# Optimization experiments

Measured on AMD Instinct MI355X. Metric: run time of the kernel, lower is better.

## Reference

```python
import jax, jax.numpy as jnp
import numpy as np

N_NODES = 20000
N_EDGES = 320000
DIMS = [256, 256, 128, 64]  # input_dim, hidden_dims...
EPS = 1e-5


def gcn_conv(x, w, b, src, dst, n):
    # PyG GCNConv: linear first, then symmetric-normalized aggregation with self-loops
    x = x @ w  # [N, out]
    loops = jnp.arange(n, dtype=src.dtype)
    src2 = jnp.concatenate([src, loops])
    dst2 = jnp.concatenate([dst, loops])
    deg = jax.ops.segment_sum(jnp.ones_like(dst2, dtype=x.dtype), dst2, num_segments=n)
    dinv = jnp.where(deg > 0, deg ** -0.5, 0.0)
    norm = dinv[src2] * dinv[dst2]  # [E+N]
    msg = x[src2] * norm[:, None]   # gathered, scaled messages
    out = jax.ops.segment_sum(msg, dst2, num_segments=n)
    return out + b


def graph_norm(x, w, b, a):
    # PyG GraphNorm over a single graph: per-feature mean/var across nodes
    mean = jnp.mean(x, axis=0)
    centered = x - a * mean
    var = jnp.mean(centered * centered, axis=0)
    return w * centered * jax.lax.rsqrt(var + EPS) + b


def layer_norm(x, w, b):
    mean = jnp.mean(x, axis=-1, keepdims=True)
    var = jnp.mean((x - mean) ** 2, axis=-1, keepdims=True)
    return (x - mean) * jax.lax.rsqrt(var + EPS) * w + b


def setup_inputs() -> dict:
    key = jax.random.key(0)
    ks = jax.random.split(key, 32)
    inp = {}
    inp["x"] = jax.random.normal(ks[0], (N_NODES, DIMS[0]), dtype=jnp.float32)
    inp["edge_index"] = jax.random.randint(ks[1], (2, N_EDGES), 0, N_NODES, dtype=jnp.int32)
    ki = 2
    for i in range(3):
        fin, fout = DIMS[i], DIMS[i + 1]
        s = 1.0 / np.sqrt(fin)
        inp[f"w{i}"] = jax.random.uniform(ks[ki], (fin, fout), jnp.float32, -s, s); ki += 1
        inp[f"b{i}"] = jnp.zeros((fout,), jnp.float32)
        inp[f"gn{i}_w"] = jnp.ones((fout,), jnp.float32)
        inp[f"gn{i}_b"] = jnp.zeros((fout,), jnp.float32)
        inp[f"gn{i}_a"] = jnp.ones((fout,), jnp.float32)
    h = DIMS[-1]
    s = 1.0 / np.sqrt(3 * h)
    inp["wc1"] = jax.random.uniform(ks[ki], (3 * h, h), jnp.float32, -s, s); ki += 1
    inp["bc1"] = jnp.zeros((h,), jnp.float32)
    inp["ln_w"] = jnp.ones((h,), jnp.float32)
    inp["ln_b"] = jnp.zeros((h,), jnp.float32)
    s = 1.0 / np.sqrt(h)
    inp["wc2"] = jax.random.uniform(ks[ki], (h, 2), jnp.float32, -s, s); ki += 1
    inp["bc2"] = jnp.zeros((2,), jnp.float32)
    return inp


def reference(x, edge_index,
              w0, b0, gn0_w, gn0_b, gn0_a,
              w1, b1, gn1_w, gn1_b, gn1_a,
              w2, b2, gn2_w, gn2_b, gn2_a,
              wc1, bc1, ln_w, ln_b, wc2, bc2):
    src, dst = edge_index[0], edge_index[1]
    n = x.shape[0]
    params = [(w0, b0, gn0_w, gn0_b, gn0_a),
              (w1, b1, gn1_w, gn1_b, gn1_a),
              (w2, b2, gn2_w, gn2_b, gn2_a)]
    for (w, b, gw, gb, ga) in params:
        x_res = x
        x = gcn_conv(x, w, b, src, dst, n)
        x = graph_norm(x, gw, gb, ga)
        x = jax.nn.gelu(x, approximate=False)
        # dropout = identity (eval); residual only when shapes match (layer 0)
        if x.shape == x_res.shape:
            x = x + x_res
    # multi-pool over the single graph (batch vector of zeros): mean | max | sum
    pooled = jnp.concatenate([jnp.mean(x, axis=0), jnp.max(x, axis=0), jnp.sum(x, axis=0)])[None, :]  # [1, 3h]
    h = pooled @ wc1 + bc1
    h = layer_norm(h, ln_w, ln_b)
    h = jax.nn.gelu(h, approximate=False)
    return h @ wc2 + bc2  # [1, num_classes]
```

## Files before the change

### kernel.cpp

```cpp
#include <hip/hip_runtime.h>
#include <math.h>

#define EPSV 1e-5f
#define MAXB 2560
#define GBLK 2080

__device__ __forceinline__ float gelu_f(float x) {
    return 0.5f * x * (1.0f + erff(x * 0.70710678118654752440f));
}

__device__ __forceinline__ float4 f4add(float4 a, float4 b) {
    return make_float4(a.x + b.x, a.y + b.y, a.z + b.z, a.w + b.w);
}

__global__ void deg_kernel(const int* __restrict__ ei, int* __restrict__ deg, int E) {
    int stride = gridDim.x * blockDim.x;
    for (int e = blockIdx.x * blockDim.x + threadIdx.x; e < E; e += stride)
        atomicAdd(&deg[ei[E + e]], 1);
}

__global__ void dinv_kernel(const int* __restrict__ deg, float* __restrict__ dinv, int N) {
    int i = blockIdx.x * blockDim.x + threadIdx.x;
    if (i < N) dinv[i] = rsqrtf((float)(deg[i] + 1));
}

__global__ __launch_bounds__(1024) void scan_kernel(const int* __restrict__ deg,
                                                    int* __restrict__ off, int N) {
    __shared__ int sh[1024];
    int t = threadIdx.x;
    int chunk = (N + 1023) >> 10;
    int b = t * chunk;
    int e = b + chunk; if (e > N) e = N;
    int s = 0;
    for (int i = b; i < e; ++i) s += deg[i];
    sh[t] = s;
    __syncthreads();
    for (int d = 1; d < 1024; d <<= 1) {
        int v = (t >= d) ? sh[t - d] : 0;
        __syncthreads();
        sh[t] += v;
        __syncthreads();
    }
    int run = (t > 0) ? sh[t - 1] : 0;
    for (int i = b; i < e; ++i) { off[i] = run; run += deg[i]; }
    if (t == 1023) off[N] = sh[1023];
}

__global__ void fill_kernel(const int* __restrict__ ei, const int* __restrict__ off,
                            int* __restrict__ fill, int* __restrict__ csr, int E) {
    int stride = gridDim.x * blockDim.x;
    for (int e = blockIdx.x * blockDim.x + threadIdx.x; e < E; e += stride) {
        int d = ei[E + e];
        int p = off[d] + atomicAdd(&fill[d], 1);
        csr[p] = ei[e];
    }
}

__global__ __launch_bounds__(256) void gemm_scale_kernel(
    const float* __restrict__ A, const float* __restrict__ W,
    const float* __restrict__ dinv, float* __restrict__ C,
    int M, int K, int Nc)
{
    __shared__ float As[64][17];
    __shared__ float4 Ws4[16][16];
    const int tid = threadIdx.x;
    const int tx = tid & 15, ty = tid >> 4;
    const int row0 = blockIdx.y * 64, col0 = blockIdx.x * 64;
    float acc[4][4] = {};
    const int ar = tid >> 2, ac4 = (tid & 3) * 4;
    const int wr = tid >> 4, wc4 = (tid & 15) * 4;

    for (int kk = 0; kk < K; kk += 16) {
        float4 av = make_float4(0.f, 0.f, 0.f, 0.f);
        int grow = row0 + ar;
        if (grow < M) av = *(const float4*)(A + (long)grow * K + kk + ac4);
        As[ar][ac4 + 0] = av.x; As[ar][ac4 + 1] = av.y;
        As[ar][ac4 + 2] = av.z; As[ar][ac4 + 3] = av.w;
        Ws4[wr][tid & 15] = *(const float4*)(W + (long)(kk + wr) * Nc + col0 + wc4);
        __syncthreads();
#pragma unroll
        for (int k = 0; k < 16; ++k) {
            float4 b4 = Ws4[k][tx];
            float a0 = As[ty * 4 + 0][k];
            float a1 = As[ty * 4 + 1][k];
            float a2 = As[ty * 4 + 2][k];
            float a3 = As[ty * 4 + 3][k];
            acc[0][0] = fmaf(a0, b4.x, acc[0][0]); acc[0][1] = fmaf(a0, b4.y, acc[0][1]);
            acc[0][2] = fmaf(a0, b4.z, acc[0][2]); acc[0][3] = fmaf(a0, b4.w, acc[0][3]);
            acc[1][0] = fmaf(a1, b4.x, acc[1][0]); acc[1][1] = fmaf(a1, b4.y, acc[1][1]);
            acc[1][2] = fmaf(a1, b4.z, acc[1][2]); acc[1][3] = fmaf(a1, b4.w, acc[1][3]);
            acc[2][0] = fmaf(a2, b4.x, acc[2][0]); acc[2][1] = fmaf(a2, b4.y, acc[2][1]);
            acc[2][2] = fmaf(a2, b4.z, acc[2][2]); acc[2][3] = fmaf(a2, b4.w, acc[2][3]);
            acc[3][0] = fmaf(a3, b4.x, acc[3][0]); acc[3][1] = fmaf(a3, b4.y, acc[3][1]);
            acc[3][2] = fmaf(a3, b4.z, acc[3][2]); acc[3][3] = fmaf(a3, b4.w, acc[3][3]);
        }
        __syncthreads();
    }
#pragma unroll
    for (int i = 0; i < 4; ++i) {
        int grow = row0 + ty * 4 + i;
        if (grow < M) {
            float dv = dinv[grow];
            float4 o = make_float4(acc[i][0] * dv, acc[i][1] * dv, acc[i][2] * dv, acc[i][3] * dv);
            *(float4*)(C + (long)grow * Nc + col0 + tx * 4) = o;
        }
    }
}

template<int F>
__global__ __launch_bounds__(256) void gather_kernel(
    const float* __restrict__ hs, const int* __restrict__ off,
    const int* __restrict__ csr, const float* __restrict__ dinv,
    const float* __restrict__ bias, float* __restrict__ t,
    float* __restrict__ p1, float* __restrict__ p2, int N)
{
    constexpr int NG  = F / 64;
    constexpr int LDR = F / 4;
    constexpr int NPB = 16;
    const int lane = threadIdx.x & 15;
    const int slot = threadIdx.x >> 4;

    const int xs    = blockIdx.x & 7;
    const int g     = xs % NG;
    const int r     = xs / NG;
    const int chunk = blockIdx.x >> 3;
    const int repl  = 8 / NG;
    const int nPerG = (int)(gridDim.x >> 3) * repl;
    const int j     = chunk * repl + r;

    const int col4 = g * 16 + lane;
    const float4* hs4 = (const float4*)hs;
    float4* t4 = (float4*)t;
    const float4 bv = ((const float4*)bias)[col4];

    float4 a1 = make_float4(0.f, 0.f, 0.f, 0.f);
    float4 a2 = make_float4(0.f, 0.f, 0.f, 0.f);

    for (int d = j * NPB + slot; d < N; d += nPerG * NPB) {
        float4 acc = hs4[(long)d * LDR + col4];
        const int e0 = off[d], e1 = off[d + 1];
        int e = e0;
        for (; e + 8 <= e1; e += 8) {
            int s0 = csr[e + 0], s1 = csr[e + 1], s2 = csr[e + 2], s3 = csr[e + 3];
            int s4 = csr[e + 4], s5 = csr[e + 5], s6 = csr[e + 6], s7 = csr[e + 7];
            float4 v0 = hs4[(long)s0 * LDR + col4];
            float4 v1 = hs4[(long)s1 * LDR + col4];
            float4 v2 = hs4[(long)s2 * LDR + col4];
            float4 v3 = hs4[(long)s3 * LDR + col4];
            float4 v4 = hs4[(long)s4 * LDR + col4];
            float4 v5 = hs4[(long)s5 * LDR + col4];
            float4 v6 = hs4[(long)s6 * LDR + col4];
            float4 v7 = hs4[(long)s7 * LDR + col4];
            float4 u0 = f4add(v0, v1);
            float4 u1 = f4add(v2, v3);
            float4 u2 = f4add(v4, v5);
            float4 u3 = f4add(v6, v7);
            acc = f4add(acc, f4add(f4add(u0, u1), f4add(u2, u3)));
        }
        for (; e + 2 <= e1; e += 2) {
            int s0 = csr[e + 0], s1 = csr[e + 1];
            acc = f4add(acc, f4add(hs4[(long)s0 * LDR + col4], hs4[(long)s1 * LDR + col4]));
        }
        if (e < e1) {
            acc = f4add(acc, hs4[(long)csr[e] * LDR + col4]);
        }

        float dv = dinv[d];
        float4 o;
        o.x = fmaf(dv, acc.x, bv.x);
        o.y = fmaf(dv, acc.y, bv.y);
        o.z = fmaf(dv, acc.z, bv.z);
        o.w = fmaf(dv, acc.w, bv.w);
        t4[(long)d * LDR + col4] = o;
        a1.x += o.x; a1.y += o.y; a1.z += o.z; a1.w += o.w;
        a2.x += o.x * o.x; a2.y += o.y * o.y; a2.z += o.z * o.z; a2.w += o.w * o.w;
    }

    __shared__ float red[8][256];
    red[0][threadIdx.x] = a1.x; red[1][threadIdx.x] = a1.y;
    red[2][threadIdx.x] = a1.z; red[3][threadIdx.x] = a1.w;
    red[4][threadIdx.x] = a2.x; red[5][threadIdx.x] = a2.y;
    red[6][threadIdx.x] = a2.z; red[7][threadIdx.x] = a2.w;
    __syncthreads();
    if (slot == 0) {
        float sum[8];
#pragma unroll
        for (int k = 0; k < 8; ++k) {
            float s = red[k][lane];
            for (int jj = 1; jj < NPB; ++jj) s += red[k][jj * 16 + lane];
            sum[k] = s;
        }
        ((float4*)p1)[(long)col4 * MAXB + blockIdx.x] = make_float4(sum[0], sum[1], sum[2], sum[3]);
        ((float4*)p2)[(long)col4 * MAXB + blockIdx.x] = make_float4(sum[4], sum[5], sum[6], sum[7]);
    }
}

__global__ __launch_bounds__(256) void statreduce_kernel(
    const float* __restrict__ p1, const float* __restrict__ p2,
    const float* __restrict__ ga,
    float* __restrict__ meanv, float* __restrict__ istdv,
    int nb, int N, int NG)
{
    const int c4 = blockIdx.x;
    const int g = (c4 >> 4) % NG;
    const float4* p14 = (const float4*)p1 + (long)c4 * MAXB;
    const float4* p24 = (const float4*)p2 + (long)c4 * MAXB;
    float4 a1 = make_float4(0.f, 0.f, 0.f, 0.f);
    float4 a2 = make_float4(0.f, 0.f, 0.f, 0.f);
    for (int r = threadIdx.x; r < nb; r += 256) {
        if (((r & 7) % NG) != g) continue;
        float4 v1 = p14[r];
        float4 v2 = p24[r];
        a1.x += v1.x; a1.y += v1.y; a1.z += v1.z; a1.w += v1.w;
        a2.x += v2.x; a2.y += v2.y; a2.z += v2.z; a2.w += v2.w;
    }
#pragma unroll
    for (int offv = 32; offv > 0; offv >>= 1) {
        a1.x += __shfl_down(a1.x, offv); a1.y += __shfl_down(a1.y, offv);
        a1.z += __shfl_down(a1.z, offv); a1.w += __shfl_down(a1.w, offv);
        a2.x += __shfl_down(a2.x, offv); a2.y += __shfl_down(a2.y, offv);
        a2.z += __shfl_down(a2.z, offv); a2.w += __shfl_down(a2.w, offv);
    }
    __shared__ float4 sh1[4], sh2[4];
    const int wid = threadIdx.x >> 6;
    if ((threadIdx.x & 63) == 0) { sh1[wid] = a1; sh2[wid] = a2; }
    __syncthreads();
    if (threadIdx.x == 0) {
        float4 t1 = sh1[0], t2 = sh2[0];
        for (int jj = 1; jj < 4; ++jj) {
            float4 u1 = sh1[jj], u2 = sh2[jj];
            t1.x += u1.x; t1.y += u1.y; t1.z += u1.z; t1.w += u1.w;
            t2.x += u2.x; t2.y += u2.y; t2.z += u2.z; t2.w += u2.w;
        }
        float s1a[4] = { t1.x, t1.y, t1.z, t1.w };
        float s2a[4] = { t2.x, t2.y, t2.z, t2.w };
#pragma unroll
        for (int k = 0; k < 4; ++k) {
            int c = c4 * 4 + k;
            float m = s1a[k] / (float)N;
            float a = ga[c];
            float var = s2a[k] / (float)N - 2.f * a * m * m + a * a * m * m;
            meanv[c] = m;
            istdv[c] = rsqrtf(var + EPSV);
        }
    }
}

__global__ __launch_bounds__(256) void normgelu_kernel(
    const float* __restrict__ t, const float* __restrict__ meanv,
    const float* __restrict__ istdv, const float* __restrict__ gw,
    const float* __restrict__ gb, const float* __restrict__ ga,
    const float* __restrict__ res, float* __restrict__ out,
    int log2f, long total)
{
    long stride = (long)gridDim.x * blockDim.x;
    int fmask = (1 << log2f) - 1;
    for (long idx = (long)blockIdx.x * blockDim.x + threadIdx.x; idx < total; idx += stride) {
        int c = (int)idx & fmask;
        float v = t[idx];
        float y = gw[c] * (v - ga[c] * meanv[c]) * istdv[c] + gb[c];
        y = gelu_f(y);
        if (res) y += res[idx];
        out[idx] = y;
    }
}

__device__ __forceinline__ void atomicMaxFloat(float* addr, float val) {
    unsigned* ua = (unsigned*)addr;
    unsigned old = *ua;
    while (true) {
        float of = __uint_as_float(old);
        if (of >= val) break;
        unsigned assumed = old;
        old = atomicCAS(ua, assumed, __float_as_uint(val));
        if (old == assumed) break;
    }
}

__global__ void initpool_kernel(float* __restrict__ psum, float* __restrict__ pmax) {
    int t = threadIdx.x;
    psum[t] = 0.f;
    pmax[t] = -INFINITY;
}

__global__ __launch_bounds__(256) void colpool_kernel(
    const float* __restrict__ x, float* __restrict__ psum, float* __restrict__ pmax,
    int M, int rowsPerBlock)
{
    int c = threadIdx.x & 63;
    int rl = threadIdx.x >> 6;
    int r0 = blockIdx.x * rowsPerBlock;
    int rend = r0 + rowsPerBlock; if (rend > M) rend = M;
    float a1 = 0.f, am = -INFINITY;
    for (int r = r0 + rl; r < rend; r += 4) {
        float v = x[(long)r * 64 + c];
        a1 += v; am = fmaxf(am, v);
    }
    __shared__ float sh1[256], shm[256];
    sh1[threadIdx.x] = a1; shm[threadIdx.x] = am;
    __syncthreads();
    if (threadIdx.x < 64) {
        for (int j = 1; j < 4; ++j) {
            a1 += sh1[c + j * 64];
            am = fmaxf(am, shm[c + j * 64]);
        }
        atomicAdd(&psum[c], a1);
        atomicMaxFloat(&pmax[c], am);
    }
}

__global__ void head_kernel(const float* __restrict__ psum, const float* __restrict__ pmax,
                            const float* __restrict__ wc1, const float* __restrict__ bc1,
                            const float* __restrict__ lnw, const float* __restrict__ lnb,
                            const float* __restrict__ wc2, const float* __restrict__ bc2,
                            float* __restrict__ out, int M)
{
    __shared__ float p[192];
    int t = threadIdx.x;
    float s = psum[t];
    p[t] = s / (float)M;
    p[64 + t] = pmax[t];
    p[128 + t] = s;
    __syncthreads();
    float h = bc1[t];
    for (int k = 0; k < 192; ++k) h = fmaf(p[k], wc1[k * 64 + t], h);
    float m = h;
    for (int off = 32; off > 0; off >>= 1) m += __shfl_xor(m, off);
    m *= (1.f / 64.f);
    float d = h - m;
    float v = d * d;
    for (int off = 32; off > 0; off >>= 1) v += __shfl_xor(v, off);
    v *= (1.f / 64.f);
    float y = d * rsqrtf(v + EPSV) * lnw[t] + lnb[t];
    y = gelu_f(y);
    float o0 = y * wc2[t * 2 + 0];
    float o1 = y * wc2[t * 2 + 1];
    for (int off = 32; off > 0; off >>= 1) {
        o0 += __shfl_xor(o0, off);
        o1 += __shfl_xor(o1, off);
    }
    if (t == 0) {
        out[0] = o0 + bc2[0];
        out[1] = o1 + bc2[1];
    }
}

extern "C" void kernel_launch(void* const* d_in, const int* in_sizes, int n_in,
                              void* d_out, int out_size, void* d_ws, size_t ws_size,
                              hipStream_t stream)
{
    const float* x    = (const float*)d_in[0];
    const int*   ei   = (const int*)d_in[1];
    const float* w0   = (const float*)d_in[2];
    const float* b0   = (const float*)d_in[3];
    const float* gn0w = (const float*)d_in[4];
    const float* gn0b = (const float*)d_in[5];
    const float* gn0a = (const float*)d_in[6];
    const float* w1   = (const float*)d_in[7];
    const float* b1   = (const float*)d_in[8];
    const float* gn1w = (const float*)d_in[9];
    const float* gn1b = (const float*)d_in[10];
    const float* gn1a = (const float*)d_in[11];
    const float* w2   = (const float*)d_in[12];
    const float* b2   = (const float*)d_in[13];
    const float* gn2w = (const float*)d_in[14];
    const float* gn2b = (const float*)d_in[15];
    const float* gn2a = (const float*)d_in[16];
    const float* wc1  = (const float*)d_in[17];
    const float* bc1  = (const float*)d_in[18];
    const float* lnw  = (const float*)d_in[19];
    const float* lnb  = (const float*)d_in[20];
    const float* wc2  = (const float*)d_in[21];
    const float* bc2  = (const float*)d_in[22];

    const int N = in_sizes[0] / 256;
    const int E = in_sizes[1] / 2;

    float* ws = (float*)d_ws;
    const size_t BIG = (size_t)N * 256;
    float* BUF0  = ws;
    float* BUF1  = ws + BIG;
    float* dinv  = ws + 2 * BIG;
    int*   deg   = (int*)(dinv + N);
    int*   off   = deg + N;
    int*   fill  = off + N + 1;
    int*   csr   = fill + N;
    float* p1    = (float*)(csr + E);
    float* p2    = p1 + (size_t)MAXB * 256;
    float* meanv = p2 + (size_t)MAXB * 256;
    float* istdv = meanv + 256;
    float* psum  = istdv + 256;
    float* pmax  = psum + 64;

    hipMemsetAsync(deg, 0, (size_t)N * sizeof(int), stream);
    hipMemsetAsync(fill, 0, (size_t)N * sizeof(int), stream);
    deg_kernel<<<1024, 256, 0, stream>>>(ei, deg, E);
    dinv_kernel<<<(N + 255) / 256, 256, 0, stream>>>(deg, dinv, N);
    scan_kernel<<<1, 1024, 0, stream>>>(deg, off, N);
    fill_kernel<<<1024, 256, 0, stream>>>(ei, off, fill, csr, E);

    struct Layer {
        const float *w, *b, *gw, *gb, *ga;
        int K, F, lf;
    } L[3] = {
        { w0, b0, gn0w, gn0b, gn0a, 256, 256, 8 },
        { w1, b1, gn1w, gn1b, gn1a, 256, 128, 7 },
        { w2, b2, gn2w, gn2b, gn2a, 128,  64, 6 },
    };
    const float* resb[3] = { x, nullptr, nullptr };

    const float* cur = x;
    for (int li = 0; li < 3; ++li) {
        const int K = L[li].K, F = L[li].F, lf = L[li].lf;
        const long total = (long)N << lf;
        dim3 gg(F / 64, (N + 63) / 64);
        gemm_scale_kernel<<<gg, 256, 0, stream>>>(cur, L[li].w, dinv, BUF0, N, K, F);

        if (F == 256) {
            gather_kernel<256><<<GBLK, 256, 0, stream>>>(BUF0, off, csr, dinv, L[li].b, BUF1, p1, p2, N);
        } else if (F == 128) {
            gather_kernel<128><<<GBLK, 256, 0, stream>>>(BUF0, off, csr, dinv, L[li].b, BUF1, p1, p2, N);
        } else {
            gather_kernel<64><<<GBLK, 256, 0, stream>>>(BUF0, off, csr, dinv, L[li].b, BUF1, p1, p2, N);
        }
        statreduce_kernel<<<F / 4, 256, 0, stream>>>(p1, p2, L[li].ga, meanv, istdv, GBLK, N, F / 64);

        long fb = (total + 255) / 256; if (fb > 4096) fb = 4096;
        normgelu_kernel<<<(int)fb, 256, 0, stream>>>(BUF1, meanv, istdv,
                                                     L[li].gw, L[li].gb, L[li].ga,
                                                     resb[li], BUF1, lf, total);
        cur = BUF1;
    }

    initpool_kernel<<<1, 64, 0, stream>>>(psum, pmax);
    colpool_kernel<<<(N + 127) / 128, 256, 0, stream>>>(cur, psum, pmax, N, 128);
    head_kernel<<<1, 64, 0, stream>>>(psum, pmax, wc1, bc1, lnw, lnb, wc2, bc2,
                                      (float*)d_out, N);
}
```

Before: 318.4 us.

## Replace FP32 SIMT GEMM with split-bf16 MFMA GEMM and bf16 activation packing

The scalar FP32 tiled GEMM is replaced by a matrix-core kernel that uses bf16 MFMA with a three-term hi/lo split (hi*hi + hi*lo + lo*hi) to keep close to FP32 accuracy. Input features and per-layer outputs are stored as hi/lo bf16 pairs by a new pack kernel and by the norm+GELU epilogue. Weights are packed and transposed by a small kernel each layer. This trades three MFMA passes, extra pack launches and no LDS staging (operands are read straight from global memory) for much higher matrix throughput. The GEMM writes its output as scattered scalar stores, and the buffers now ping-pong between layers.

```diff
diff --git a/kernel.cpp b/kernel.cpp
--- a/kernel.cpp
+++ b/kernel.cpp
@@ -2,8 +2,11 @@
 #include <math.h>
 
 #define EPSV 1e-5f
-#define MAXB 2560
+#define MAXB 2176
 #define GBLK 2080
+
+typedef __attribute__((ext_vector_type(8))) short short8;
+typedef __attribute__((ext_vector_type(4))) float f32x4;
 
 __device__ __forceinline__ float gelu_f(float x) {
     return 0.5f * x * (1.0f + erff(x * 0.70710678118654752440f));
@@ -11,6 +14,16 @@
 
 __device__ __forceinline__ float4 f4add(float4 a, float4 b) {
     return make_float4(a.x + b.x, a.y + b.y, a.z + b.z, a.w + b.w);
+}
+
+__device__ __forceinline__ ushort f2bf(float v) {
+    union { float f; unsigned u; } a; a.f = v;
+    unsigned r = a.u + 0x7FFFu + ((a.u >> 16) & 1u);
+    return (ushort)(r >> 16);
+}
+__device__ __forceinline__ float bf2f(ushort h) {
+    union { unsigned u; float f; } a; a.u = ((unsigned)h) << 16;
+    return a.f;
 }
 
 __global__ void deg_kernel(const int* __restrict__ ei, int* __restrict__ deg, int E) {
@@ -56,53 +69,81 @@
     }
 }
 
-__global__ __launch_bounds__(256) void gemm_scale_kernel(
-    const float* __restrict__ A, const float* __restrict__ W,
+__global__ __launch_bounds__(256) void packx_kernel(
+    const float* __restrict__ x, ushort* __restrict__ hi, ushort* __restrict__ lo, long n)
+{
+    long stride = (long)gridDim.x * blockDim.x * 4;
+    for (long i = ((long)blockIdx.x * blockDim.x + threadIdx.x) * 4; i < n; i += stride) {
+        float4 v = *(const float4*)(x + i);
+        ushort4 h, l2;
+        h.x = f2bf(v.x); h.y = f2bf(v.y); h.z = f2bf(v.z); h.w = f2bf(v.w);
+        l2.x = f2bf(v.x - bf2f(h.x)); l2.y = f2bf(v.y - bf2f(h.y));
+        l2.z = f2bf(v.z - bf2f(h.z)); l2.w = f2bf(v.w - bf2f(h.w));
+        *(ushort4*)(hi + i) = h;
+        *(ushort4*)(lo + i) = l2;
+    }
+}
+
+__global__ void packw_kernel(const float* __restrict__ W, ushort* __restrict__ wthi,
+                             ushort* __restrict__ wtlo, int K, int F)
+{
+    int idx = blockIdx.x * 256 + threadIdx.x;
+    if (idx >= K * F) return;
+    int k = idx / F, f = idx - k * F;
+    float v = W[idx];
+    ushort h = f2bf(v);
+    wthi[f * K + k] = h;
+    wtlo[f * K + k] = f2bf(v - bf2f(h));
+}
+
+template<int K>
+__global__ __launch_bounds__(256) void gemm_mfma_kernel(
+    const ushort* __restrict__ ahi, const ushort* __restrict__ alo,
+    const ushort* __restrict__ wthi, const ushort* __restrict__ wtlo,
     const float* __restrict__ dinv, float* __restrict__ C,
-    int M, int K, int Nc)
-{
-    __shared__ float As[64][17];
-    __shared__ float4 Ws4[16][16];
-    const int tid = threadIdx.x;
-    const int tx = tid & 15, ty = tid >> 4;
-    const int row0 = blockIdx.y * 64, col0 = blockIdx.x * 64;
-    float acc[4][4] = {};
-    const int ar = tid >> 2, ac4 = (tid & 3) * 4;
-    const int wr = tid >> 4, wc4 = (tid & 15) * 4;
-
-    for (int kk = 0; kk < K; kk += 16) {
-        float4 av = make_float4(0.f, 0.f, 0.f, 0.f);
-        int grow = row0 + ar;
-        if (grow < M) av = *(const float4*)(A + (long)grow * K + kk + ac4);
-        As[ar][ac4 + 0] = av.x; As[ar][ac4 + 1] = av.y;
-        As[ar][ac4 + 2] = av.z; As[ar][ac4 + 3] = av.w;
-        Ws4[wr][tid & 15] = *(const float4*)(W + (long)(kk + wr) * Nc + col0 + wc4);
-        __syncthreads();
+    int M, int F)
+{
+    const int l  = threadIdx.x & 63;
+    const int w  = threadIdx.x >> 6;
+    const int row0 = blockIdx.y * 64 + w * 16;
+    const int col0 = blockIdx.x * 64;
+    const int lr = l & 15;
+    const int lk = (l >> 4) * 8;
+
+    int arow = row0 + lr; if (arow > M - 1) arow = M - 1;
+
+    f32x4 acc0 = {}, acc1 = {}, acc2 = {}, acc3 = {};
+
+    const ushort* aA[3] = { ahi, ahi, alo };
+    const ushort* wW[3] = { wthi, wtlo, wthi };
 #pragma unroll
-        for (int k = 0; k < 16; ++k) {
-            float4 b4 = Ws4[k][tx];
-            float a0 = As[ty * 4 + 0][k];
-            float a1 = As[ty * 4 + 1][k];
-            float a2 = As[ty * 4 + 2][k];
-            float a3 = As[ty * 4 + 3][k];
-            acc[0][0] = fmaf(a0, b4.x, acc[0][0]); acc[0][1] = fmaf(a0, b4.y, acc[0][1]);
-            acc[0][2] = fmaf(a0, b4.z, acc[0][2]); acc[0][3] = fmaf(a0, b4.w, acc[0][3]);
-            acc[1][0] = fmaf(a1, b4.x, acc[1][0]); acc[1][1] = fmaf(a1, b4.y, acc[1][1]);
-            acc[1][2] = fmaf(a1, b4.z, acc[1][2]); acc[1][3] = fmaf(a1, b4.w, acc[1][3]);
-            acc[2][0] = fmaf(a2, b4.x, acc[2][0]); acc[2][1] = fmaf(a2, b4.y, acc[2][1]);
-            acc[2][2] = fmaf(a2, b4.z, acc[2][2]); acc[2][3] = fmaf(a2, b4.w, acc[2][3]);
-            acc[3][0] = fmaf(a3, b4.x, acc[3][0]); acc[3][1] = fmaf(a3, b4.y, acc[3][1]);
-            acc[3][2] = fmaf(a3, b4.z, acc[3][2]); acc[3][3] = fmaf(a3, b4.w, acc[3][3]);
-        }
-        __syncthreads();
-    }
+    for (int s = 0; s < 3; ++s) {
+        const ushort* Ap = aA[s] + (size_t)arow * K + lk;
+        const ushort* Wp = wW[s] + (size_t)(col0 + lr) * K + lk;
+        for (int kk = 0; kk < K; kk += 32) {
+            short8 af = *(const short8*)(Ap + kk);
+            short8 b0 = *(const short8*)(Wp + kk);
+            short8 b1 = *(const short8*)(Wp + 16 * K + kk);
+            short8 b2 = *(const short8*)(Wp + 32 * K + kk);
+            short8 b3 = *(const short8*)(Wp + 48 * K + kk);
+            acc0 = __builtin_amdgcn_mfma_f32_16x16x32_bf16(af, b0, acc0, 0, 0, 0);
+            acc1 = __builtin_amdgcn_mfma_f32_16x16x32_bf16(af, b1, acc1, 0, 0, 0);
+            acc2 = __builtin_amdgcn_mfma_f32_16x16x32_bf16(af, b2, acc2, 0, 0, 0);
+            acc3 = __builtin_amdgcn_mfma_f32_16x16x32_bf16(af, b3, acc3, 0, 0, 0);
+        }
+    }
+
+    const int rbase = row0 + (l >> 4) * 4;
 #pragma unroll
-    for (int i = 0; i < 4; ++i) {
-        int grow = row0 + ty * 4 + i;
-        if (grow < M) {
-            float dv = dinv[grow];
-            float4 o = make_float4(acc[i][0] * dv, acc[i][1] * dv, acc[i][2] * dv, acc[i][3] * dv);
-            *(float4*)(C + (long)grow * Nc + col0 + tx * 4) = o;
+    for (int j = 0; j < 4; ++j) {
+        int r = rbase + j;
+        if (r < M) {
+            float dvv = dinv[r];
+            float* Cp = C + (size_t)r * F + col0 + lr;
+            Cp[0]  = acc0[j] * dvv;
+            Cp[16] = acc1[j] * dvv;
+            Cp[32] = acc2[j] * dvv;
+            Cp[48] = acc3[j] * dvv;
         }
     }
 }
@@ -250,7 +291,9 @@
     const float* __restrict__ t, const float* __restrict__ meanv,
     const float* __restrict__ istdv, const float* __restrict__ gw,
     const float* __restrict__ gb, const float* __restrict__ ga,
-    const float* __restrict__ res, float* __restrict__ out,
+    const float* __restrict__ res,
+    ushort* __restrict__ ohi, ushort* __restrict__ olo,
+    float* __restrict__ fpout,
     int log2f, long total)
 {
     long stride = (long)gridDim.x * blockDim.x;
@@ -261,7 +304,13 @@
         float y = gw[c] * (v - ga[c] * meanv[c]) * istdv[c] + gb[c];
         y = gelu_f(y);
         if (res) y += res[idx];
-        out[idx] = y;
+        if (ohi) {
+            ushort h = f2bf(y);
+            ohi[idx] = h;
+            olo[idx] = f2bf(y - bf2f(h));
+        } else {
+            fpout[idx] = y;
+        }
     }
 }
 
@@ -378,19 +427,21 @@
 
     float* ws = (float*)d_ws;
     const size_t BIG = (size_t)N * 256;
-    float* BUF0  = ws;
-    float* BUF1  = ws + BIG;
+    float* B0    = ws;
+    float* B1    = ws + BIG;
     float* dinv  = ws + 2 * BIG;
     int*   deg   = (int*)(dinv + N);
     int*   off   = deg + N;
     int*   fill  = off + N + 1;
     int*   csr   = fill + N;
     float* p1    = (float*)(csr + E);
-    float* p2    = p1 + (size_t)MAXB * 256;
-    float* meanv = p2 + (size_t)MAXB * 256;
+    float* p2    = p1 + (size_t)64 * MAXB * 4;
+    float* meanv = p2 + (size_t)64 * MAXB * 4;
     float* istdv = meanv + 256;
     float* psum  = istdv + 256;
     float* pmax  = psum + 64;
+    ushort* wthi = (ushort*)(pmax + 64);
+    ushort* wtlo = wthi + 256 * 256;
 
     hipMemsetAsync(deg, 0, (size_t)N * sizeof(int), stream);
     hipMemsetAsync(fill, 0, (size_t)N * sizeof(int), stream);
@@ -398,6 +449,8 @@
     dinv_kernel<<<(N + 255) / 256, 256, 0, stream>>>(deg, dinv, N);
     scan_kernel<<<1, 1024, 0, stream>>>(deg, off, N);
     fill_kernel<<<1024, 256, 0, stream>>>(ei, off, fill, csr, E);
+
+    packx_kernel<<<1280, 256, 0, stream>>>(x, (ushort*)B0, (ushort*)B0 + BIG, (long)BIG);
 
     struct Layer {
         const float *w, *b, *gw, *gb, *ga;
@@ -408,32 +461,47 @@
         { w2, b2, gn2w, gn2b, gn2a, 128,  64, 6 },
     };
     const float* resb[3] = { x, nullptr, nullptr };
-
-    const float* cur = x;
+    float* Bb[2] = { B0, B1 };
+
+    int cur = 0;
     for (int li = 0; li < 3; ++li) {
         const int K = L[li].K, F = L[li].F, lf = L[li].lf;
         const long total = (long)N << lf;
+        float* Ab = Bb[cur];
+        float* HS = Bb[cur ^ 1];
+        ushort* ahi = (ushort*)Ab;
+        ushort* alo = ahi + BIG;
+
+        packw_kernel<<<(K * F + 255) / 256, 256, 0, stream>>>(L[li].w, wthi, wtlo, K, F);
+
         dim3 gg(F / 64, (N + 63) / 64);
-        gemm_scale_kernel<<<gg, 256, 0, stream>>>(cur, L[li].w, dinv, BUF0, N, K, F);
-
-        if (F == 256) {
-            gather_kernel<256><<<GBLK, 256, 0, stream>>>(BUF0, off, csr, dinv, L[li].b, BUF1, p1, p2, N);
-        } else if (F == 128) {
-            gather_kernel<128><<<GBLK, 256, 0, stream>>>(BUF0, off, csr, dinv, L[li].b, BUF1, p1, p2, N);
-        } else {
-            gather_kernel<64><<<GBLK, 256, 0, stream>>>(BUF0, off, csr, dinv, L[li].b, BUF1, p1, p2, N);
-        }
+        if (K == 256)
+            gemm_mfma_kernel<256><<<gg, 256, 0, stream>>>(ahi, alo, wthi, wtlo, dinv, HS, N, F);
+        else
+            gemm_mfma_kernel<128><<<gg, 256, 0, stream>>>(ahi, alo, wthi, wtlo, dinv, HS, N, F);
+
+        float* T = Ab;
+        if (F == 256)
+            gather_kernel<256><<<GBLK, 256, 0, stream>>>(HS, off, csr, dinv, L[li].b, T, p1, p2, N);
+        else if (F == 128)
+            gather_kernel<128><<<GBLK, 256, 0, stream>>>(HS, off, csr, dinv, L[li].b, T, p1, p2, N);
+        else
+            gather_kernel<64><<<GBLK, 256, 0, stream>>>(HS, off, csr, dinv, L[li].b, T, p1, p2, N);
+
         statreduce_kernel<<<F / 4, 256, 0, stream>>>(p1, p2, L[li].ga, meanv, istdv, GBLK, N, F / 64);
 
         long fb = (total + 255) / 256; if (fb > 4096) fb = 4096;
-        normgelu_kernel<<<(int)fb, 256, 0, stream>>>(BUF1, meanv, istdv,
+        ushort* ohi = (li < 2) ? (ushort*)HS : nullptr;
+        ushort* olo = (li < 2) ? (ushort*)HS + BIG : nullptr;
+        float*  fpo = (li == 2) ? HS : nullptr;
+        normgelu_kernel<<<(int)fb, 256, 0, stream>>>(T, meanv, istdv,
                                                      L[li].gw, L[li].gb, L[li].ga,
-                                                     resb[li], BUF1, lf, total);
-        cur = BUF1;
+                                                     resb[li], ohi, olo, fpo, lf, total);
+        cur ^= 1;
     }
 
     initpool_kernel<<<1, 64, 0, stream>>>(psum, pmax);
-    colpool_kernel<<<(N + 127) / 128, 256, 0, stream>>>(cur, psum, pmax, N, 128);
+    colpool_kernel<<<(N + 127) / 128, 256, 0, stream>>>(Bb[cur], psum, pmax, N, 128);
     head_kernel<<<1, 64, 0, stream>>>(psum, pmax, wc1, bc1, lnw, lnb, wc2, bc2,
                                       (float*)d_out, N);
 }
```

Result: slower. 346.4 us (+8.8%).
